# Kernel optimization log

Hardware: AMD Instinct MI355X
Metric: run time of the kernel (lower is better)

Reference implementation:

```python
import jax, jax.numpy as jnp
import numpy as np

B, T, D, H, HD, I = 256, 1, 2048, 16, 128, 5504
EPS = 1e-6
ROPE_THETA = 10000.0


def setup_inputs() -> dict:
    key = jax.random.key(0)
    ks = jax.random.split(key, 20)
    W = 0.02  # weight init scale
    hidden_states = jax.random.normal(ks[0], (B, T, D), jnp.float32)
    # RoPE tables for each batch element at a distinct decode position
    pos = jnp.arange(B, dtype=jnp.float32) % 4096.0
    inv_freq = 1.0 / (ROPE_THETA ** (jnp.arange(0, HD, 2, dtype=jnp.float32) / HD))
    ang = pos[:, None] * inv_freq[None, :]                      # [B, HD/2]
    emb = jnp.concatenate([ang, ang], axis=-1)                  # [B, HD]
    cos = jnp.cos(emb)[:, None, :]                              # [B, 1, HD]
    sin = jnp.sin(emb)[:, None, :]
    n = lambda k, s: jax.random.normal(k, s, jnp.float32) * W
    return {
        'hidden_states': hidden_states, 'cos': cos, 'sin': sin,
        'router_w': n(ks[1], (D,)), 'router_b': jnp.zeros((1,), jnp.float32),
        'ln1_w': jnp.ones((D,), jnp.float32), 'ln2_w': jnp.ones((D,), jnp.float32),
        'wq': n(ks[2], (D, D)), 'bq': jnp.zeros((D,), jnp.float32),
        'wk': n(ks[3], (D, D)), 'bk': jnp.zeros((D,), jnp.float32),
        'wv': n(ks[4], (D, D)), 'bv': jnp.zeros((D,), jnp.float32),
        'wo': n(ks[5], (D, D)),
        'w_gate': n(ks[6], (D, I)), 'w_up': n(ks[7], (D, I)), 'w_down': n(ks[8], (I, D)),
        'k_sel': 128,
    }


def _rms(x, w):
    v = jnp.mean(jnp.square(x), axis=-1, keepdims=True)
    return x * jax.lax.rsqrt(v + EPS) * w


def _rotate_half(x):
    x1, x2 = jnp.split(x, 2, axis=-1)
    return jnp.concatenate([-x2, x1], axis=-1)


def _decoder_layer(x, cs, sn, ln1_w, ln2_w, wq, bq, wk, bk, wv, bv, wo, w_gate, w_up, w_down):
    # x: [k, T, D]; cs/sn: [k, T, HD]
    k = x.shape[0]
    h = _rms(x, ln1_w)
    q = (h @ wq + bq).reshape(k, T, H, HD).transpose(0, 2, 1, 3)  # [k,H,T,HD]
    kk = (h @ wk + bk).reshape(k, T, H, HD).transpose(0, 2, 1, 3)
    v = (h @ wv + bv).reshape(k, T, H, HD).transpose(0, 2, 1, 3)
    c = cs[:, None, :, :]  # [k,1,T,HD]
    s = sn[:, None, :, :]
    q = q * c + _rotate_half(q) * s
    kk = kk * c + _rotate_half(kk) * s
    att = jnp.einsum('bhqd,bhkd->bhqk', q, kk) * (HD ** -0.5)
    p = jax.nn.softmax(att, axis=-1)  # T==1: trivial causal mask
    o = jnp.einsum('bhqk,bhkd->bhqd', p, v).transpose(0, 2, 1, 3).reshape(k, T, D) @ wo
    x = x + o
    h2 = _rms(x, ln2_w)
    mlp = (jax.nn.silu(h2 @ w_gate) * (h2 @ w_up)) @ w_down
    return x + mlp


def reference(hidden_states, cos, sin, router_w, router_b, ln1_w, ln2_w,
              wq, bq, wk, bk, wv, bv, wo, w_gate, w_up, w_down, k_sel):
    # causal router: linear D->1 scores per batch row (T==1 decode step)
    scores = hidden_states[:, 0, :] @ router_w + router_b[0]   # [B]
    probs = jax.nn.sigmoid(scores)
    _, sel_idx = jax.lax.top_k(probs, k_sel)                   # [k]
    x_sel = hidden_states[sel_idx]                             # gather [k,T,D]
    cs, sn = cos[sel_idx], sin[sel_idx]                        # [k,T,HD]
    x_out = _decoder_layer(x_sel, cs, sn, ln1_w, ln2_w, wq, bq, wk, bk,
                           wv, bv, wo, w_gate, w_up, w_down)
    return hidden_states.at[sel_idx].set(x_out)                # scatter back
```

## Files before the change

kernel.cpp:

```cpp
#include <hip/hip_runtime.h>
#include <hip/hip_bf16.h>
#include <stdint.h>


#define D_ 2048
#define I_ 5504
#define NROWS 256
#define KSEL 128

typedef __attribute__((ext_vector_type(8))) short short8;
typedef __attribute__((ext_vector_type(4))) float floatx4;

__device__ __forceinline__ unsigned int pk2(float lo, float hi) {
  __hip_bfloat162 h = __float22bfloat162_rn(float2{lo, hi});
  unsigned int u; __builtin_memcpy(&u, &h, 4); return u;
}

__global__ void k_zero(float4* __restrict__ p, int n4) {
  int i = blockIdx.x * 256 + threadIdx.x;
  int st = gridDim.x * 256;
  for (; i < n4; i += st) p[i] = float4{0.f, 0.f, 0.f, 0.f};
}

__global__ void k_router(const float* __restrict__ hid, const float* __restrict__ rw,
                         const float* __restrict__ rb, float* __restrict__ scores) {
  int b = blockIdx.x, t = threadIdx.x;
  const float4* x4 = (const float4*)(hid + (size_t)b * D_);
  const float4* w4 = (const float4*)rw;
  float s = 0.f;
#pragma unroll
  for (int c = 0; c < 2; ++c) {
    float4 xv = x4[t + c * 256], wv = w4[t + c * 256];
    s += xv.x * wv.x + xv.y * wv.y + xv.z * wv.z + xv.w * wv.w;
  }
  for (int o = 32; o; o >>= 1) s += __shfl_down(s, o);
  __shared__ float red[4];
  if ((t & 63) == 0) red[t >> 6] = s;
  __syncthreads();
  if (t == 0) scores[b] = red[0] + red[1] + red[2] + red[3] + rb[0];
}

__global__ void k_select(const float* __restrict__ scores, const int* __restrict__ kptr,
                         int* __restrict__ sel, int* __restrict__ pos) {
  __shared__ float sv[NROWS];
  int t = threadIdx.x;
  sv[t] = scores[t];
  __syncthreads();
  float s = sv[t];
  int c = 0;
  for (int j = 0; j < NROWS; ++j) {
    float o = sv[j];
    c += (o > s) || (o == s && j < t);
  }
  int k = *kptr;
  if (c < k) sel[c] = t;
  pos[t] = (c < k) ? c : -1;
}

__global__ void k_rms1(const float* __restrict__ hid, const int* __restrict__ sel,
                       const float* __restrict__ ln1, const float* __restrict__ bv,
                       unsigned short* __restrict__ Hb, float* __restrict__ V,
                       float* __restrict__ X1) {
  int i = blockIdx.x, t = threadIdx.x;
  int r = sel[i];
  const float4* x4 = (const float4*)(hid + (size_t)r * D_);
  float4 xa = x4[2 * t], xb = x4[2 * t + 1];
  float ss = xa.x * xa.x + xa.y * xa.y + xa.z * xa.z + xa.w * xa.w
           + xb.x * xb.x + xb.y * xb.y + xb.z * xb.z + xb.w * xb.w;
  for (int o = 32; o; o >>= 1) ss += __shfl_down(ss, o);
  __shared__ float red[4];
  if ((t & 63) == 0) red[t >> 6] = ss;
  __syncthreads();
  float inv = rsqrtf((red[0] + red[1] + red[2] + red[3]) * (1.0f / D_) + 1e-6f);
  const float4* w4 = (const float4*)ln1;
  float4 wa = w4[2 * t], wb = w4[2 * t + 1];
  union { unsigned int u[4]; uint4 q; } pk;
  pk.u[0] = pk2(xa.x * inv * wa.x, xa.y * inv * wa.y);
  pk.u[1] = pk2(xa.z * inv * wa.z, xa.w * inv * wa.w);
  pk.u[2] = pk2(xb.x * inv * wb.x, xb.y * inv * wb.y);
  pk.u[3] = pk2(xb.z * inv * wb.z, xb.w * inv * wb.w);
  ((uint4*)(Hb + (size_t)i * D_))[t] = pk.q;
  const float4* b4 = (const float4*)bv;
  float4* V4 = (float4*)(V + (size_t)i * D_);
  V4[2 * t] = b4[2 * t]; V4[2 * t + 1] = b4[2 * t + 1];
  float4* X4 = (float4*)(X1 + (size_t)i * D_);
  X4[2 * t] = xa; X4[2 * t + 1] = xb;
}

__global__ void k_rms2(const float* __restrict__ X1, const float* __restrict__ ln2,
                       unsigned short* __restrict__ H2b) {
  int i = blockIdx.x, t = threadIdx.x;
  const float4* x4 = (const float4*)(X1 + (size_t)i * D_);
  float4 xa = x4[2 * t], xb = x4[2 * t + 1];
  float ss = xa.x * xa.x + xa.y * xa.y + xa.z * xa.z + xa.w * xa.w
           + xb.x * xb.x + xb.y * xb.y + xb.z * xb.z + xb.w * xb.w;
  for (int o = 32; o; o >>= 1) ss += __shfl_down(ss, o);
  __shared__ float red[4];
  if ((t & 63) == 0) red[t >> 6] = ss;
  __syncthreads();
  float inv = rsqrtf((red[0] + red[1] + red[2] + red[3]) * (1.0f / D_) + 1e-6f);
  const float4* w4 = (const float4*)ln2;
  float4 wa = w4[2 * t], wb = w4[2 * t + 1];
  union { unsigned int u[4]; uint4 q; } pk;
  pk.u[0] = pk2(xa.x * inv * wa.x, xa.y * inv * wa.y);
  pk.u[1] = pk2(xa.z * inv * wa.z, xa.w * inv * wa.w);
  pk.u[2] = pk2(xb.x * inv * wb.x, xb.y * inv * wb.y);
  pk.u[3] = pk2(xb.z * inv * wb.z, xb.w * inv * wb.w);
  ((uint4*)(H2b + (size_t)i * D_))[t] = pk.q;
}

__global__ void k_silu_out(const float* __restrict__ G, const float* __restrict__ U,
                           unsigned short* __restrict__ Mb,
                           const float* __restrict__ X1, const int* __restrict__ pos,
                           const float* __restrict__ hid, float* __restrict__ out) {
  int tid = blockIdx.x * 256 + threadIdx.x;
  const int nM4 = KSEL * I_ / 4;
  if (tid < nM4) {
    float4 g = ((const float4*)G)[tid], u = ((const float4*)U)[tid];
    float m0 = (g.x / (1.f + expf(-g.x))) * u.x;
    float m1 = (g.y / (1.f + expf(-g.y))) * u.y;
    float m2 = (g.z / (1.f + expf(-g.z))) * u.z;
    float m3 = (g.w / (1.f + expf(-g.w))) * u.w;
    uint2 o; o.x = pk2(m0, m1); o.y = pk2(m2, m3);
    ((uint2*)Mb)[tid] = o;
  }
  const int nO4 = NROWS * (D_ / 4);
  if (tid < nO4) {
    int row = tid >> 9;
    int c4 = tid & 511;
    int p = pos[row];
    ((float4*)out)[tid] = (p >= 0) ? ((const float4*)X1)[(size_t)p * 512 + c4]
                                   : ((const float4*)hid)[tid];
  }
}

template<bool AF32, bool DUAL>
__global__ __launch_bounds__(256, 4)
void k_gemm(const void* __restrict__ Ap, const float* __restrict__ B0,
            const float* __restrict__ B1, float* __restrict__ C0,
            float* __restrict__ C1, const int* __restrict__ rowmap,
            int K, int KA, int Kb, int lda, int N, int KT, int ldc) {
  constexpr int ST = 72;
  const int bn = blockIdx.x;
  const int kt0 = blockIdx.y * KT;
  const int kt1 = kt0 + KT;
  const int tid = threadIdx.x;
  const int lane = tid & 63;
  const int wave = tid >> 6;
  const int wm = wave >> 1, wn = wave & 1;
  const int fm = lane & 15, kq = lane >> 4;

  __shared__ alignas(16) unsigned short Asm[128 * ST];
  __shared__ alignas(16) unsigned short Bsm0[32 * ST];
  __shared__ alignas(16) unsigned short Bsm1[DUAL ? 32 * ST : 8];

  floatx4 acc0[4] = {};
  floatx4 acc1[4] = {};

  const int arow = tid >> 3;
  const int akg  = (tid & 7) * 8;
  const int frow = tid >> 4;
  const int fkg  = (tid & 15) * 4;
  const int bnn = tid & 31;
  const int bk8 = (tid >> 5) * 8;

  const unsigned short* Ab = AF32 ? nullptr : (const unsigned short*)Ap;
  const float*          Af = AF32 ? (const float*)Ap : nullptr;
  const float* B0c = B0 + (size_t)(bn * 32 + bnn);
  const float* B1c = DUAL ? B1 + (size_t)(bn * 32 + bnn) : nullptr;

  uint4 a4[4];
  float4 af8[8];
  float b0v[8], b1v[8];

  auto load_tile = [&](int kt) {
    if (AF32) {
      const int c0 = kt + fkg;
      const bool ok = c0 < KA;
#pragma unroll
      for (int r = 0; r < 8; ++r) {
        const float* p = Af + (size_t)(r * 16 + frow) * lda + c0;
        af8[r] = ok ? *(const float4*)p : make_float4(0.f, 0.f, 0.f, 0.f);
      }
    } else {
      const int c0 = kt + akg;
      const bool ok = c0 < KA;
#pragma unroll
      for (int r = 0; r < 4; ++r) {
        const unsigned short* p = Ab + (size_t)(r * 32 + arow) * lda + c0;
        a4[r] = ok ? *(const uint4*)p : make_uint4(0u, 0u, 0u, 0u);
      }
    }
#pragma unroll
    for (int j = 0; j < 8; ++j) {
      int kr = kt + bk8 + j; kr = kr < Kb ? kr : Kb - 1;
      b0v[j] = B0c[(size_t)kr * N];
      if (DUAL) b1v[j] = B1c[(size_t)kr * N];
    }
  };

  load_tile(kt0);

  for (int kt = kt0; kt < kt1; kt += 64) {
    __syncthreads();
    {
      if (AF32) {
#pragma unroll
        for (int r = 0; r < 8; ++r) {
          uint2 w;
          w.x = pk2(af8[r].x, af8[r].y);
          w.y = pk2(af8[r].z, af8[r].w);
          *(uint2*)&Asm[(r * 16 + frow) * ST + fkg] = w;
        }
      } else {
#pragma unroll
        for (int r = 0; r < 4; ++r)
          *(uint4*)&Asm[(r * 32 + arow) * ST + akg] = a4[r];
      }
      uint4 bq;
      bq.x = pk2(b0v[0], b0v[1]); bq.y = pk2(b0v[2], b0v[3]);
      bq.z = pk2(b0v[4], b0v[5]); bq.w = pk2(b0v[6], b0v[7]);
      *(uint4*)&Bsm0[bnn * ST + bk8] = bq;
      if (DUAL) {
        uint4 cq;
        cq.x = pk2(b1v[0], b1v[1]); cq.y = pk2(b1v[2], b1v[3]);
        cq.z = pk2(b1v[4], b1v[5]); cq.w = pk2(b1v[6], b1v[7]);
        *(uint4*)&Bsm1[bnn * ST + bk8] = cq;
      }
    }
    __syncthreads();
    if (kt + 64 < kt1) load_tile(kt + 64);
    short8 afr[2][4], bf0[2], bf1[2];
#pragma unroll
    for (int s = 0; s < 2; ++s) {
#pragma unroll
      for (int i = 0; i < 4; ++i)
        afr[s][i] = *(const short8*)&Asm[(wm * 64 + i * 16 + fm) * ST + s * 32 + kq * 8];
      bf0[s] = *(const short8*)&Bsm0[(wn * 16 + fm) * ST + s * 32 + kq * 8];
      if (DUAL)
        bf1[s] = *(const short8*)&Bsm1[(wn * 16 + fm) * ST + s * 32 + kq * 8];
    }
#pragma unroll
    for (int s = 0; s < 2; ++s) {
#pragma unroll
      for (int i = 0; i < 4; ++i) {
        acc0[i] = __builtin_amdgcn_mfma_f32_16x16x32_bf16(afr[s][i], bf0[s], acc0[i], 0, 0, 0);
        if (DUAL)
          acc1[i] = __builtin_amdgcn_mfma_f32_16x16x32_bf16(afr[s][i], bf1[s], acc1[i], 0, 0, 0);
      }
    }
  }

#pragma unroll
  for (int i = 0; i < 4; ++i) {
#pragma unroll
    for (int r = 0; r < 4; ++r) {
      int row = wm * 64 + i * 16 + kq * 4 + r;
      size_t rbase = rowmap ? (size_t)rowmap[row] * ldc : (size_t)row * ldc;
      int col = bn * 32 + wn * 16 + fm;
      atomicAdd(&C0[rbase + col], acc0[i][r]);
      if (DUAL) atomicAdd(&C1[rbase + col], acc1[i][r]);
    }
  }
}

extern "C" void kernel_launch(void* const* d_in, const int* in_sizes, int n_in,
                              void* d_out, int out_size, void* d_ws, size_t ws_size,
                              hipStream_t stream) {
  const float* hid = (const float*)d_in[0];
  const float* rw  = (const float*)d_in[3];
  const float* rb  = (const float*)d_in[4];
  const float* ln1 = (const float*)d_in[5];
  const float* ln2 = (const float*)d_in[6];
  const float* wv  = (const float*)d_in[11];
  const float* bv  = (const float*)d_in[12];
  const float* wo  = (const float*)d_in[13];
  const float* wg  = (const float*)d_in[14];
  const float* wu  = (const float*)d_in[15];
  const float* wd  = (const float*)d_in[16];
  const int*   kp  = (const int*)d_in[17];
  float* out = (float*)d_out;

  char* ws = (char*)d_ws;
  float*          scores = (float*)(ws + 0);
  int*            sel    = (int*)(ws + 1024);
  int*            pos    = (int*)(ws + 1536);
  unsigned short* Hb     = (unsigned short*)(ws + 4096);
  float*          V      = (float*)(ws + 528384);
  float*          X1     = (float*)(ws + 1576960);
  unsigned short* H2b    = (unsigned short*)(ws + 2625536);
  float*          G      = (float*)(ws + 3149824);
  float*          U      = (float*)(ws + 5967872);
  unsigned short* Mb     = (unsigned short*)(ws + 8785920);

  k_zero<<<1024, 256, 0, stream>>>((float4*)G, 352256);
  k_router<<<256, 256, 0, stream>>>(hid, rw, rb, scores);
  k_select<<<1, 256, 0, stream>>>(scores, kp, sel, pos);
  k_rms1<<<128, 256, 0, stream>>>(hid, sel, ln1, bv, Hb, V, X1);
  k_gemm<false, false><<<dim3(64, 16), 256, 0, stream>>>(
      Hb, wv, nullptr, V, nullptr, nullptr, 2048, 2048, 2048, 2048, 2048, 128, 2048);
  k_gemm<true, false><<<dim3(64, 16), 256, 0, stream>>>(
      V, wo, nullptr, X1, nullptr, nullptr, 2048, 2048, 2048, 2048, 2048, 128, 2048);
  k_rms2<<<128, 256, 0, stream>>>(X1, ln2, H2b);
  k_gemm<false, true><<<dim3(172, 8), 256, 0, stream>>>(
      H2b, wg, wu, G, U, nullptr, 2048, 2048, 2048, 2048, 5504, 256, 5504);
  k_silu_out<<<1024, 256, 0, stream>>>(G, U, Mb, X1, pos, hid, out);
  k_gemm<false, false><<<dim3(64, 16), 256, 0, stream>>>(
      Mb, wd, nullptr, out, nullptr, sel, 6144, 5504, 5504, 5504, 2048, 384, 2048);
}
```

Measured before the change: 309.1 us.

## Double-buffer GEMM register prefetch two tiles ahead and halve split-K

```diff
diff --git a/kernel.cpp b/kernel.cpp
--- a/kernel.cpp
+++ b/kernel.cpp
@@ -135,7 +135,7 @@
 }
 
 template<bool AF32, bool DUAL>
-__global__ __launch_bounds__(256, 4)
+__global__ __launch_bounds__(256, 2)
 void k_gemm(const void* __restrict__ Ap, const float* __restrict__ B0,
             const float* __restrict__ B1, float* __restrict__ C0,
             float* __restrict__ C1, const int* __restrict__ rowmap,
@@ -169,18 +169,20 @@
   const float* B0c = B0 + (size_t)(bn * 32 + bnn);
   const float* B1c = DUAL ? B1 + (size_t)(bn * 32 + bnn) : nullptr;
 
-  uint4 a4[4];
-  float4 af8[8];
-  float b0v[8], b1v[8];
-
-  auto load_tile = [&](int kt) {
-    if (AF32) {
+  struct Regs {
+    uint4 a4[4];
+    float4 af8[8];
+    float b0v[8], b1v[8];
+  };
+
+  auto load_tile = [&](Regs& R, int kt) {
+    if constexpr (AF32) {
       const int c0 = kt + fkg;
       const bool ok = c0 < KA;
 #pragma unroll
       for (int r = 0; r < 8; ++r) {
         const float* p = Af + (size_t)(r * 16 + frow) * lda + c0;
-        af8[r] = ok ? *(const float4*)p : make_float4(0.f, 0.f, 0.f, 0.f);
+        R.af8[r] = ok ? *(const float4*)p : make_float4(0.f, 0.f, 0.f, 0.f);
       }
     } else {
       const int c0 = kt + akg;
@@ -188,48 +190,44 @@
 #pragma unroll
       for (int r = 0; r < 4; ++r) {
         const unsigned short* p = Ab + (size_t)(r * 32 + arow) * lda + c0;
-        a4[r] = ok ? *(const uint4*)p : make_uint4(0u, 0u, 0u, 0u);
+        R.a4[r] = ok ? *(const uint4*)p : make_uint4(0u, 0u, 0u, 0u);
       }
     }
 #pragma unroll
     for (int j = 0; j < 8; ++j) {
       int kr = kt + bk8 + j; kr = kr < Kb ? kr : Kb - 1;
-      b0v[j] = B0c[(size_t)kr * N];
-      if (DUAL) b1v[j] = B1c[(size_t)kr * N];
-    }
-  };
-
-  load_tile(kt0);
-
-  for (int kt = kt0; kt < kt1; kt += 64) {
-    __syncthreads();
-    {
-      if (AF32) {
-#pragma unroll
-        for (int r = 0; r < 8; ++r) {
-          uint2 w;
-          w.x = pk2(af8[r].x, af8[r].y);
-          w.y = pk2(af8[r].z, af8[r].w);
-          *(uint2*)&Asm[(r * 16 + frow) * ST + fkg] = w;
-        }
-      } else {
-#pragma unroll
-        for (int r = 0; r < 4; ++r)
-          *(uint4*)&Asm[(r * 32 + arow) * ST + akg] = a4[r];
+      R.b0v[j] = B0c[(size_t)kr * N];
+      if constexpr (DUAL) R.b1v[j] = B1c[(size_t)kr * N];
+    }
+  };
+
+  auto store_lds = [&](Regs& R) {
+    if constexpr (AF32) {
+#pragma unroll
+      for (int r = 0; r < 8; ++r) {
+        uint2 w;
+        w.x = pk2(R.af8[r].x, R.af8[r].y);
+        w.y = pk2(R.af8[r].z, R.af8[r].w);
+        *(uint2*)&Asm[(r * 16 + frow) * ST + fkg] = w;
       }
-      uint4 bq;
-      bq.x = pk2(b0v[0], b0v[1]); bq.y = pk2(b0v[2], b0v[3]);
-      bq.z = pk2(b0v[4], b0v[5]); bq.w = pk2(b0v[6], b0v[7]);
-      *(uint4*)&Bsm0[bnn * ST + bk8] = bq;
-      if (DUAL) {
-        uint4 cq;
-        cq.x = pk2(b1v[0], b1v[1]); cq.y = pk2(b1v[2], b1v[3]);
-        cq.z = pk2(b1v[4], b1v[5]); cq.w = pk2(b1v[6], b1v[7]);
-        *(uint4*)&Bsm1[bnn * ST + bk8] = cq;
-      }
-    }
-    __syncthreads();
-    if (kt + 64 < kt1) load_tile(kt + 64);
+    } else {
+#pragma unroll
+      for (int r = 0; r < 4; ++r)
+        *(uint4*)&Asm[(r * 32 + arow) * ST + akg] = R.a4[r];
+    }
+    uint4 bq;
+    bq.x = pk2(R.b0v[0], R.b0v[1]); bq.y = pk2(R.b0v[2], R.b0v[3]);
+    bq.z = pk2(R.b0v[4], R.b0v[5]); bq.w = pk2(R.b0v[6], R.b0v[7]);
+    *(uint4*)&Bsm0[bnn * ST + bk8] = bq;
+    if constexpr (DUAL) {
+      uint4 cq;
+      cq.x = pk2(R.b1v[0], R.b1v[1]); cq.y = pk2(R.b1v[2], R.b1v[3]);
+      cq.z = pk2(R.b1v[4], R.b1v[5]); cq.w = pk2(R.b1v[6], R.b1v[7]);
+      *(uint4*)&Bsm1[bnn * ST + bk8] = cq;
+    }
+  };
+
+  auto mfma_phase = [&]() {
     short8 afr[2][4], bf0[2], bf1[2];
 #pragma unroll
     for (int s = 0; s < 2; ++s) {
@@ -237,7 +235,7 @@
       for (int i = 0; i < 4; ++i)
         afr[s][i] = *(const short8*)&Asm[(wm * 64 + i * 16 + fm) * ST + s * 32 + kq * 8];
       bf0[s] = *(const short8*)&Bsm0[(wn * 16 + fm) * ST + s * 32 + kq * 8];
-      if (DUAL)
+      if constexpr (DUAL)
         bf1[s] = *(const short8*)&Bsm1[(wn * 16 + fm) * ST + s * 32 + kq * 8];
     }
 #pragma unroll
@@ -245,10 +243,34 @@
 #pragma unroll
       for (int i = 0; i < 4; ++i) {
         acc0[i] = __builtin_amdgcn_mfma_f32_16x16x32_bf16(afr[s][i], bf0[s], acc0[i], 0, 0, 0);
-        if (DUAL)
+        if constexpr (DUAL)
           acc1[i] = __builtin_amdgcn_mfma_f32_16x16x32_bf16(afr[s][i], bf1[s], acc1[i], 0, 0, 0);
       }
     }
+  };
+
+  auto stage = [&](Regs& R, int kt) {
+    __builtin_amdgcn_s_barrier();
+    __builtin_amdgcn_sched_barrier(0);
+    store_lds(R);
+    if (kt + 128 < kt1) load_tile(R, kt + 128);
+    asm volatile("s_waitcnt lgkmcnt(0)" ::: "memory");
+    __builtin_amdgcn_s_barrier();
+    __builtin_amdgcn_sched_barrier(0);
+    mfma_phase();
+    __builtin_amdgcn_sched_barrier(0);
+  };
+
+  Regs ra, rb;
+  load_tile(ra, kt0);
+  load_tile(rb, kt0 + 64);
+
+  int kt = kt0;
+  while (true) {
+    stage(ra, kt);
+    kt += 64; if (kt >= kt1) break;
+    stage(rb, kt);
+    kt += 64; if (kt >= kt1) break;
   }
 
 #pragma unroll
@@ -259,7 +281,7 @@
       size_t rbase = rowmap ? (size_t)rowmap[row] * ldc : (size_t)row * ldc;
       int col = bn * 32 + wn * 16 + fm;
       atomicAdd(&C0[rbase + col], acc0[i][r]);
-      if (DUAL) atomicAdd(&C1[rbase + col], acc1[i][r]);
+      if constexpr (DUAL) atomicAdd(&C1[rbase + col], acc1[i][r]);
     }
   }
 }
@@ -297,14 +319,14 @@
   k_router<<<256, 256, 0, stream>>>(hid, rw, rb, scores);
   k_select<<<1, 256, 0, stream>>>(scores, kp, sel, pos);
   k_rms1<<<128, 256, 0, stream>>>(hid, sel, ln1, bv, Hb, V, X1);
-  k_gemm<false, false><<<dim3(64, 16), 256, 0, stream>>>(
-      Hb, wv, nullptr, V, nullptr, nullptr, 2048, 2048, 2048, 2048, 2048, 128, 2048);
-  k_gemm<true, false><<<dim3(64, 16), 256, 0, stream>>>(
-      V, wo, nullptr, X1, nullptr, nullptr, 2048, 2048, 2048, 2048, 2048, 128, 2048);
+  k_gemm<false, false><<<dim3(64, 8), 256, 0, stream>>>(
+      Hb, wv, nullptr, V, nullptr, nullptr, 2048, 2048, 2048, 2048, 2048, 256, 2048);
+  k_gemm<true, false><<<dim3(64, 8), 256, 0, stream>>>(
+      V, wo, nullptr, X1, nullptr, nullptr, 2048, 2048, 2048, 2048, 2048, 256, 2048);
   k_rms2<<<128, 256, 0, stream>>>(X1, ln2, H2b);
-  k_gemm<false, true><<<dim3(172, 8), 256, 0, stream>>>(
-      H2b, wg, wu, G, U, nullptr, 2048, 2048, 2048, 2048, 5504, 256, 5504);
+  k_gemm<false, true><<<dim3(172, 4), 256, 0, stream>>>(
+      H2b, wg, wu, G, U, nullptr, 2048, 2048, 2048, 2048, 5504, 512, 5504);
   k_silu_out<<<1024, 256, 0, stream>>>(G, U, Mb, X1, pos, hid, out);
-  k_gemm<false, false><<<dim3(64, 16), 256, 0, stream>>>(
-      Mb, wd, nullptr, out, nullptr, sel, 6144, 5504, 5504, 5504, 2048, 384, 2048);
-}
+  k_gemm<false, false><<<dim3(64, 8), 256, 0, stream>>>(
+      Mb, wd, nullptr, out, nullptr, sel, 5632, 5504, 5504, 5504, 2048, 704, 2048);
+}
```

After: 287.5 us. 7.0% less time.
